# Optimization experiments

Hardware: AMD Instinct MI355X
Metric: run time of the kernel (lower is better)

## Reference

```python
import jax, jax.numpy as jnp
import numpy as np

DIM = 512
HID = 2048
E = 16
B = 8
N = 2048
THRESHOLD = 0.8
CAP_FACTOR = 2.0  # eval mode
MIN_EXPERT_CAPACITY = 4
LOSS_COEF = 0.01
CAP = max(MIN_EXPERT_CAPACITY, min(N, int(N * CAP_FACTOR / E)))  # 256


def setup_inputs() -> dict:
    key = jax.random.key(0)
    k1, k2, k3, k4 = jax.random.split(key, 4)
    x = jax.random.normal(k1, (B, N, DIM), dtype=jnp.float32)
    w_gating = jax.random.normal(k2, (DIM, E), dtype=jnp.float32)
    std1 = 1.0 / np.sqrt(HID)
    std2 = 1.0 / np.sqrt(DIM)
    w1 = jax.random.uniform(k3, (E, DIM, HID), jnp.float32, -std1, std1)
    w2 = jax.random.uniform(k4, (E, HID, DIM), jnp.float32, -std2, std2)
    return {"x": x, "w_gating": w_gating, "w1": w1, "w2": w2}


def _gate(x, w_gating):
    # raw gate probabilities [B, N, E]
    raw = jax.nn.softmax(jnp.einsum('bnd,de->bne', x, w_gating), axis=-1)
    order = jnp.argsort(-raw, axis=-1)                      # descending sort indices
    sp = jnp.take_along_axis(raw, order, axis=-1)           # sorted probs (desc)
    cum = jnp.cumsum(sp, axis=-1)
    tm = cum >= THRESHOLD
    k = jnp.argmax(tm.astype(jnp.float32), axis=-1) + 1     # dynamic k per token
    k = jnp.where(jnp.any(tm, axis=-1), k, E)
    # select top-k in sorted order, renormalize
    rank = jnp.arange(E)
    sel = (rank < k[..., None]).astype(raw.dtype)           # [B,N,E] sorted order
    selp = sp * sel
    normp = selp / jnp.sum(selp, axis=-1, keepdims=True)
    # scatter back to expert order via inverse permutation
    inv = jnp.argsort(order, axis=-1)
    mask = jnp.take_along_axis(sel, inv, axis=-1)           # expert_masks [B,N,E]
    weights = jnp.take_along_axis(normp, inv, axis=-1)      # expert_weights
    # capacity: exclusive cumsum over tokens
    pos = (jnp.cumsum(mask, axis=-2) - mask) * mask
    mask = mask * (pos < float(CAP)).astype(mask.dtype)
    pos = pos * mask
    pos_tok = jnp.sum(pos, axis=-1).astype(jnp.int32)       # [B,N] (summed across experts, as in source)
    in_cap = (pos_tok < CAP).astype(raw.dtype)
    oh = jax.nn.one_hot(pos_tok, CAP, dtype=raw.dtype) * in_cap[..., None]  # [B,N,CAP]
    dispatch = mask[..., None] * oh[..., None, :]           # [B,N,E,CAP]
    combine = (weights * mask)[..., None] * oh[..., None, :]
    density = jnp.mean(mask, axis=-2)
    density_proxy = jnp.mean(raw, axis=-2)
    loss = jnp.mean(density_proxy * density) * float(E * E)
    loss = loss + 0.0 * jnp.mean(k.astype(jnp.float32))
    return dispatch, combine, loss


def reference(x, w_gating, w1, w2):
    dispatch, combine, loss = _gate(x, w_gating)
    expert_inputs = jnp.einsum('bnd,bnec->ebcd', x, dispatch)        # [E,B,CAP,D]
    ei = expert_inputs.reshape(E, B * CAP, DIM)
    hidden = jax.nn.gelu(jnp.einsum('end,edh->enh', ei, w1), approximate=False)
    eo = jnp.einsum('enh,ehd->end', hidden, w2).reshape(E, B, CAP, DIM)
    output = jnp.einsum('ebcd,bnec->bnd', eo, combine)               # [B,N,D]
    return output, loss * LOSS_COEF
```

## Files before the change

kernel.cpp:

```cpp
#include <hip/hip_runtime.h>
#include <math.h>

#define DIMC 512
#define HIDC 2048
#define EC   16
#define BC   8
#define NC   2048
#define CAPC 256
#define BN   (BC * NC)
#define THRESH 0.8f

typedef unsigned short u16;
typedef __attribute__((ext_vector_type(8))) __bf16 bf16x8;
typedef __attribute__((ext_vector_type(4))) float f32x4;

__device__ __forceinline__ float bf2f(u16 u) {
    union { unsigned i; float f; } v; v.i = ((unsigned)u) << 16; return v.f;
}
__device__ __forceinline__ u16 f2bf(float f) {
    union { float f; unsigned i; } v; v.f = f;
    unsigned r = v.i + 0x7fff + ((v.i >> 16) & 1);
    return (u16)(r >> 16);
}

__global__ __launch_bounds__(64) void gate_kernel(const float* __restrict__ x,
                                                  const float* __restrict__ wg,
                                                  float* __restrict__ raw,
                                                  float* __restrict__ weights,
                                                  float* __restrict__ maskf)
{
    int token = blockIdx.x;
    int lane  = threadIdx.x;
    const float* xr = x + (size_t)token * DIMC;

    float acc[EC];
#pragma unroll
    for (int e = 0; e < EC; ++e) acc[e] = 0.f;
#pragma unroll
    for (int j = 0; j < 8; ++j) {
        int d = lane * 8 + j;
        float xv = xr[d];
        const float* wrow = wg + (size_t)d * EC;
#pragma unroll
        for (int e = 0; e < EC; ++e) acc[e] += xv * wrow[e];
    }
#pragma unroll
    for (int e = 0; e < EC; ++e) {
#pragma unroll
        for (int off = 32; off >= 1; off >>= 1)
            acc[e] += __shfl_xor(acc[e], off);
    }
    float logit = acc[0];
#pragma unroll
    for (int e = 1; e < EC; ++e)
        if (lane == e) logit = acc[e];

    float m = logit;
#pragma unroll
    for (int off = 8; off >= 1; off >>= 1) m = fmaxf(m, __shfl_xor(m, off, 16));
    float p = expf(logit - m);
    float s = p;
#pragma unroll
    for (int off = 8; off >= 1; off >>= 1) s += __shfl_xor(s, off, 16);
    p = p / s;

    int lane16 = lane & 15;
    int   rank = 0;
    float cum  = p;
#pragma unroll
    for (int j = 1; j < 16; ++j) {
        float op  = __shfl_xor(p, j, 16);
        int  oidx = lane16 ^ j;
        bool ahead = (op > p) || (op == p && oidx < lane16);
        if (ahead) { rank++; cum += op; }
    }
    bool tm = (cum >= THRESH);
    int kr = tm ? rank : (EC - 1);
#pragma unroll
    for (int off = 8; off >= 1; off >>= 1) kr = min(kr, __shfl_xor(kr, off, 16));
    bool sel = (rank <= kr);

    float dsel = sel ? p : 0.f;
    float denom = dsel;
#pragma unroll
    for (int off = 8; off >= 1; off >>= 1) denom += __shfl_xor(denom, off, 16);
    float w = sel ? (p / denom) : 0.f;

    if (lane < EC) {
        size_t o = (size_t)token * EC + lane;
        raw[o]     = p;
        weights[o] = w;
        maskf[o]   = sel ? 1.f : 0.f;
    }
}

__global__ __launch_bounds__(64) void capacity_kernel(const float* __restrict__ raw,
                                                      float* __restrict__ maskf,
                                                      int* __restrict__ pos,
                                                      float* __restrict__ density,
                                                      float* __restrict__ proxy)
{
    int t = blockIdx.x;
    int b = t / EC, e = t % EC;
    int lane = threadIdx.x;

    int count = 0;
    float rsum = 0.f;
    for (int n0 = 0; n0 < NC; n0 += 64) {
        int n = n0 + lane;
        size_t idx = ((size_t)b * NC + n) * EC + e;
        float mv = maskf[idx];
        rsum += raw[idx];
        unsigned long long bal = __ballot(mv != 0.f);
        int below = __popcll(bal & ((1ull << lane) - 1ull));
        int pval = 0;
        if (mv != 0.f) {
            pval = count + below;
            if (pval >= CAPC) { maskf[idx] = 0.f; pval = 0; }
        }
        pos[idx] = pval;
        count += __popcll(bal);
    }
#pragma unroll
    for (int off = 32; off >= 1; off >>= 1) rsum += __shfl_xor(rsum, off);
    if (lane == 0) {
        int admitted = count < CAPC ? count : CAPC;
        density[t] = (float)admitted / (float)NC;
        proxy[t]   = rsum / (float)NC;
    }
}

__global__ void postok_kernel(const int* __restrict__ pos, int* __restrict__ pos_tok)
{
    int t = blockIdx.x * blockDim.x + threadIdx.x;
    if (t >= BN) return;
    const int* pr = pos + (size_t)t * EC;
    int s = 0;
#pragma unroll
    for (int e = 0; e < EC; ++e) s += pr[e];
    pos_tok[t] = s;
}

__global__ void zero_kernel(float4* __restrict__ p, int n4)
{
    int i = blockIdx.x * blockDim.x + threadIdx.x;
    if (i < n4) p[i] = make_float4(0.f, 0.f, 0.f, 0.f);
}

__global__ __launch_bounds__(256) void scatter_kernel(const float* __restrict__ x,
                                                      const float* __restrict__ maskf,
                                                      const int* __restrict__ pos_tok,
                                                      float* __restrict__ ei)
{
    int token = blockIdx.x;
    int tid   = threadIdx.x;
    int c = pos_tok[token];
    if (c >= CAPC) return;
    int b = token / NC;
    const float* xr = x + (size_t)token * DIMC;
    float v0 = xr[tid], v1 = xr[tid + 256];
    const float* mr = maskf + (size_t)token * EC;
#pragma unroll
    for (int e = 0; e < EC; ++e) {
        if (mr[e] != 0.f) {
            float* dst = ei + (((size_t)e * BC + b) * CAPC + c) * DIMC;
            atomicAdd(dst + tid, v0);
            atomicAdd(dst + tid + 256, v1);
        }
    }
}

__global__ __launch_bounds__(256) void cvt_bf16_kernel(const float4* __restrict__ in,
                                                       u16* __restrict__ out, int n8)
{
    int i = blockIdx.x * 256 + threadIdx.x;
    if (i >= n8) return;
    float4 a = in[2 * i], b = in[2 * i + 1];
    uint4 v;
    v.x = (unsigned)f2bf(a.x) | ((unsigned)f2bf(a.y) << 16);
    v.y = (unsigned)f2bf(a.z) | ((unsigned)f2bf(a.w) << 16);
    v.z = (unsigned)f2bf(b.x) | ((unsigned)f2bf(b.y) << 16);
    v.w = (unsigned)f2bf(b.z) | ((unsigned)f2bf(b.w) << 16);
    *(uint4*)(out + (size_t)i * 8) = v;
}

__global__ __launch_bounds__(256) void transpose_cvt_kernel(const float* __restrict__ in,
                                                            u16* __restrict__ out,
                                                            int R, int C)
{
    __shared__ float tile[32][33];
    size_t eoff = (size_t)blockIdx.z * R * C;
    const float* ip = in + eoff;
    u16* op = out + eoff;
    int c0 = blockIdx.x * 32, r0 = blockIdx.y * 32;
    int tx = threadIdx.x & 31, ty = threadIdx.x >> 5;
#pragma unroll
    for (int i = 0; i < 32; i += 8)
        tile[ty + i][tx] = ip[(size_t)(r0 + ty + i) * C + c0 + tx];
    __syncthreads();
#pragma unroll
    for (int i = 0; i < 32; i += 8)
        op[(size_t)(c0 + ty + i) * R + r0 + tx] = f2bf(tile[tx][ty + i]);
}

__device__ __forceinline__ void async_cp16(const u16* g, u16* l) {
    __builtin_amdgcn_global_load_lds(
        (const __attribute__((address_space(1))) unsigned*)g,
        (__attribute__((address_space(3))) unsigned*)l, 16, 0, 0);
}

template<int GELU, int OUTBF16>
__global__ __launch_bounds__(256) void gemm_bt_kernel(
    const u16* __restrict__ A, const u16* __restrict__ Bt, void* __restrict__ Cv,
    int M, int N, int K, long sA, long sB, long sC)
{
    __shared__ __align__(16) u16 lds[2][128 * 64];
    int e = blockIdx.z;
    const u16* Ae = A + (size_t)e * sA;
    const u16* Be = Bt + (size_t)e * sB;
    int bm = blockIdx.y * 128, bn = blockIdx.x * 128;
    int t = threadIdx.x, lane = t & 63, w = t >> 6;
    int wm = (w & 1) * 64, wn = (w >> 1) * 64;
    int q = lane >> 4, m16 = lane & 15;

    f32x4 acc[4][4] = {};

    for (int k0 = 0; k0 < K; k0 += 64) {
#pragma unroll
        for (int i = 0; i < 4; ++i) {
            int l = i * 256 + t, r = l >> 3, s = l & 7, c8 = s ^ (r & 7);
            async_cp16(Ae + (size_t)(bm + r) * K + k0 + c8 * 8, &lds[0][l * 8]);
        }
#pragma unroll
        for (int i = 0; i < 4; ++i) {
            int l = i * 256 + t, r = l >> 3, s = l & 7, c8 = s ^ (r & 7);
            async_cp16(Be + (size_t)(bn + r) * K + k0 + c8 * 8, &lds[1][l * 8]);
        }
        __syncthreads();
#pragma unroll
        for (int kk = 0; kk < 64; kk += 32) {
            bf16x8 af[4], bfr[4];
#pragma unroll
            for (int mt = 0; mt < 4; ++mt) {
                int r = wm + mt * 16 + m16, c8 = (kk >> 3) + q;
                af[mt] = *(const bf16x8*)&lds[0][(r * 8 + (c8 ^ (r & 7))) * 8];
            }
#pragma unroll
            for (int nt = 0; nt < 4; ++nt) {
                int r = wn + nt * 16 + m16, c8 = (kk >> 3) + q;
                bfr[nt] = *(const bf16x8*)&lds[1][(r * 8 + (c8 ^ (r & 7))) * 8];
            }
#pragma unroll
            for (int mt = 0; mt < 4; ++mt)
#pragma unroll
                for (int nt = 0; nt < 4; ++nt)
                    acc[mt][nt] = __builtin_amdgcn_mfma_f32_16x16x32_bf16(
                        af[mt], bfr[nt], acc[mt][nt], 0, 0, 0);
        }
        __syncthreads();
    }

    size_t cbase = (size_t)e * sC;
#pragma unroll
    for (int mt = 0; mt < 4; ++mt)
#pragma unroll
        for (int nt = 0; nt < 4; ++nt)
#pragma unroll
            for (int r2 = 0; r2 < 4; ++r2) {
                int row = bm + wm + mt * 16 + q * 4 + r2;
                int col = bn + wn + nt * 16 + m16;
                float v = acc[mt][nt][r2];
                if (GELU) v = 0.5f * v * (1.f + erff(v * 0.70710678118654752f));
                if (OUTBF16) ((u16*)Cv)[cbase + (size_t)row * N + col] = f2bf(v);
                else         ((float*)Cv)[cbase + (size_t)row * N + col] = v;
            }
}

__global__ __launch_bounds__(256) void combine_kernel(const u16* __restrict__ eo,
                                                      const float* __restrict__ weights,
                                                      const float* __restrict__ maskf,
                                                      const int* __restrict__ pos_tok,
                                                      float* __restrict__ out)
{
    int token = blockIdx.x;
    int tid   = threadIdx.x;
    int b = token / NC;
    int c = pos_tok[token];
    float a0 = 0.f, a1 = 0.f;
    if (c < CAPC) {
        const float* wr = weights + (size_t)token * EC;
        const float* mr = maskf   + (size_t)token * EC;
#pragma unroll
        for (int e = 0; e < EC; ++e) {
            float wm = wr[e] * mr[e];
            if (wm != 0.f) {
                const u16* src = eo + (((size_t)e * BC + b) * CAPC + c) * DIMC;
                a0 += wm * bf2f(src[tid]);
                a1 += wm * bf2f(src[tid + 256]);
            }
        }
    }
    out[(size_t)token * DIMC + tid]       = a0;
    out[(size_t)token * DIMC + tid + 256] = a1;
}

__global__ void loss_kernel(const float* __restrict__ density,
                            const float* __restrict__ proxy,
                            float* __restrict__ out_loss)
{
    __shared__ float sh[BC * EC];
    int t = threadIdx.x;
    sh[t] = density[t] * proxy[t];
    __syncthreads();
    for (int s2 = (BC * EC) / 2; s2 >= 1; s2 >>= 1) {
        if (t < s2) sh[t] += sh[t + s2];
        __syncthreads();
    }
    if (t == 0)
        out_loss[0] = sh[0] * ((float)(EC * EC) / (float)(BC * EC)) * 0.01f;
}

extern "C" void kernel_launch(void* const* d_in, const int* in_sizes, int n_in,
                              void* d_out, int out_size, void* d_ws, size_t ws_size,
                              hipStream_t stream)
{
    const float* x  = (const float*)d_in[0];
    const float* wg = (const float*)d_in[1];
    const float* w1 = (const float*)d_in[2];
    const float* w2 = (const float*)d_in[3];
    float* out = (float*)d_out;

    char* ws = (char*)d_ws;
    size_t off = 0;
    auto alloc = [&](size_t bytes) -> void* {
        void* p = ws + off;
        off = (off + bytes + 255) & ~(size_t)255;
        return p;
    };
    float* raw      = (float*)alloc((size_t)BN * EC * 4);
    float* weights  = (float*)alloc((size_t)BN * EC * 4);
    float* maskf    = (float*)alloc((size_t)BN * EC * 4);
    int*   pos      = (int*)  alloc((size_t)BN * EC * 4);
    int*   pos_tok  = (int*)  alloc((size_t)BN * 4);
    float* density  = (float*)alloc(BC * EC * 4);
    float* proxy    = (float*)alloc(BC * EC * 4);
    float* ei_f32   = (float*)alloc((size_t)EC * BC * CAPC * DIMC * 4);
    u16*   hidden   = (u16*)ei_f32;
    u16*   ei_bf    = (u16*)alloc((size_t)EC * BC * CAPC * DIMC * 2);
    u16*   w1t      = (u16*)alloc((size_t)EC * DIMC * HIDC * 2);
    u16*   w2t      = (u16*)alloc((size_t)EC * HIDC * DIMC * 2);
    u16*   eo_bf    = (u16*)alloc((size_t)EC * BC * CAPC * DIMC * 2);

    (void)in_sizes; (void)n_in; (void)out_size; (void)ws_size;

    int n4 = EC * BC * CAPC * DIMC / 4;
    zero_kernel<<<(n4 + 255) / 256, 256, 0, stream>>>((float4*)ei_f32, n4);

    transpose_cvt_kernel<<<dim3(HIDC / 32, DIMC / 32, EC), 256, 0, stream>>>(w1, w1t, DIMC, HIDC);
    transpose_cvt_kernel<<<dim3(DIMC / 32, HIDC / 32, EC), 256, 0, stream>>>(w2, w2t, HIDC, DIMC);

    gate_kernel<<<BN, 64, 0, stream>>>(x, wg, raw, weights, maskf);
    capacity_kernel<<<BC * EC, 64, 0, stream>>>(raw, maskf, pos, density, proxy);
    postok_kernel<<<BN / 256, 256, 0, stream>>>(pos, pos_tok);
    scatter_kernel<<<BN, 256, 0, stream>>>(x, maskf, pos_tok, ei_f32);

    int n8 = EC * BC * CAPC * DIMC / 8;
    cvt_bf16_kernel<<<(n8 + 255) / 256, 256, 0, stream>>>((const float4*)ei_f32, ei_bf, n8);

    for (int g = 0; g < 2; ++g) {
        const u16* Ag  = ei_bf + (size_t)g * 8 * 2048 * 512;
        const u16* B1g = w1t   + (size_t)g * 8 * 2048 * 512;
        gemm_bt_kernel<1, 1><<<dim3(HIDC / 128, 2048 / 128, 8), 256, 0, stream>>>(
            Ag, B1g, hidden, 2048, HIDC, DIMC,
            (long)2048 * 512, (long)2048 * 512, (long)2048 * 2048);
        const u16* B2g = w2t + (size_t)g * 8 * 512 * 2048;
        u16* Eg = eo_bf + (size_t)g * 8 * 2048 * 512;
        gemm_bt_kernel<0, 1><<<dim3(DIMC / 128, 2048 / 128, 8), 256, 0, stream>>>(
            hidden, B2g, Eg, 2048, DIMC, HIDC,
            (long)2048 * 2048, (long)512 * 2048, (long)2048 * 512);
    }

    combine_kernel<<<BN, 256, 0, stream>>>(eo_bf, weights, maskf, pos_tok, out);
    loss_kernel<<<1, BC * EC, 0, stream>>>(density, proxy, out + (size_t)BN * DIMC);
}
```

Before: 549.7 us.

## Replace atomic scatter with linked-list bf16 gather and restructure gating and GEMM grouping

Splits gating into a vectorized logits kernel plus a per-thread softmax/top-k epilogue, and folds pos_tok accumulation into the capacity kernel. Replaces zeroing, fp32 atomic scatter and bf16 conversion with a per-slot linked list that gathers token rows straight into bf16 expert inputs. The GEMM precomputes load and LDS addresses, runs all experts in one launch when workspace allows, and uses a tanh-based GELU instead of erf. The tanh GELU is an approximation of the exact GELU the reference specifies and may affect accuracy.

```diff
diff --git a/kernel.cpp b/kernel.cpp
--- a/kernel.cpp
+++ b/kernel.cpp
@@ -14,89 +14,122 @@
 typedef __attribute__((ext_vector_type(8))) __bf16 bf16x8;
 typedef __attribute__((ext_vector_type(4))) float f32x4;
 
-__device__ __forceinline__ float bf2f(u16 u) {
-    union { unsigned i; float f; } v; v.i = ((unsigned)u) << 16; return v.f;
+__device__ __forceinline__ float bf2f(unsigned u) {
+    union { unsigned i; float f; } v; v.i = u << 16; return v.f;
 }
 __device__ __forceinline__ u16 f2bf(float f) {
     union { float f; unsigned i; } v; v.f = f;
     unsigned r = v.i + 0x7fff + ((v.i >> 16) & 1);
     return (u16)(r >> 16);
 }
-
-__global__ __launch_bounds__(64) void gate_kernel(const float* __restrict__ x,
-                                                  const float* __restrict__ wg,
-                                                  float* __restrict__ raw,
-                                                  float* __restrict__ weights,
-                                                  float* __restrict__ maskf)
-{
-    int token = blockIdx.x;
-    int lane  = threadIdx.x;
-    const float* xr = x + (size_t)token * DIMC;
-
-    float acc[EC];
-#pragma unroll
-    for (int e = 0; e < EC; ++e) acc[e] = 0.f;
-#pragma unroll
-    for (int j = 0; j < 8; ++j) {
-        int d = lane * 8 + j;
-        float xv = xr[d];
-        const float* wrow = wg + (size_t)d * EC;
-#pragma unroll
-        for (int e = 0; e < EC; ++e) acc[e] += xv * wrow[e];
-    }
+__device__ __forceinline__ float gelu_f(float x) {
+    float u = 0.7978845608028654f * (x + 0.044715f * x * x * x);
+    float t = __expf(2.f * u);
+    float th = 1.f - 2.f / (t + 1.f);
+    return 0.5f * x * (1.f + th);
+}
+
+__global__ void init_kernel(int* __restrict__ heads, int* __restrict__ pos_tok)
+{
+    int i = blockIdx.x * 256 + threadIdx.x;
+    if (i < EC * BC * CAPC) heads[i] = -1;
+    if (i < BN) pos_tok[i] = 0;
+}
+
+__global__ void wgt_kernel(const float* __restrict__ wg, float* __restrict__ wgt)
+{
+    int i = blockIdx.x * 256 + threadIdx.x;
+    int e = i >> 9, d = i & 511;
+    wgt[i] = wg[d * EC + e];
+}
+
+__global__ __launch_bounds__(256) void logits_kernel(const float* __restrict__ x,
+                                                     const float* __restrict__ wgt,
+                                                     float* __restrict__ logits)
+{
+    int t = threadIdx.x;
+    int token = blockIdx.x * 16 + (t >> 4);
+    int e = t & 15;
+    const float4* xr = (const float4*)(x + (size_t)token * DIMC);
+    const float4* wr = (const float4*)(wgt + (size_t)e * DIMC);
+    float acc = 0.f;
+#pragma unroll 8
+    for (int i = 0; i < DIMC / 4; ++i) {
+        float4 a = xr[i], b = wr[i];
+        acc += a.x * b.x + a.y * b.y + a.z * b.z + a.w * b.w;
+    }
+    logits[(size_t)token * EC + e] = acc;
+}
+
+__global__ __launch_bounds__(256) void gate_epi_kernel(const float* __restrict__ logits,
+                                                       float* __restrict__ raw,
+                                                       float* __restrict__ weights,
+                                                       float* __restrict__ maskf)
+{
+    int token = blockIdx.x * 256 + threadIdx.x;
+    const float4* lp = (const float4*)(logits + (size_t)token * EC);
+    float p[EC];
+    {
+        float4 v0 = lp[0], v1 = lp[1], v2 = lp[2], v3 = lp[3];
+        p[0]=v0.x; p[1]=v0.y; p[2]=v0.z; p[3]=v0.w;
+        p[4]=v1.x; p[5]=v1.y; p[6]=v1.z; p[7]=v1.w;
+        p[8]=v2.x; p[9]=v2.y; p[10]=v2.z; p[11]=v2.w;
+        p[12]=v3.x; p[13]=v3.y; p[14]=v3.z; p[15]=v3.w;
+    }
+    float m = p[0];
+#pragma unroll
+    for (int e = 1; e < EC; ++e) m = fmaxf(m, p[e]);
+    float s = 0.f;
+#pragma unroll
+    for (int e = 0; e < EC; ++e) { p[e] = expf(p[e] - m); s += p[e]; }
+    float inv = 1.f / s;
+#pragma unroll
+    for (int e = 0; e < EC; ++e) p[e] *= inv;
+
+    int rank[EC]; float cum[EC];
 #pragma unroll
     for (int e = 0; e < EC; ++e) {
-#pragma unroll
-        for (int off = 32; off >= 1; off >>= 1)
-            acc[e] += __shfl_xor(acc[e], off);
-    }
-    float logit = acc[0];
-#pragma unroll
-    for (int e = 1; e < EC; ++e)
-        if (lane == e) logit = acc[e];
-
-    float m = logit;
-#pragma unroll
-    for (int off = 8; off >= 1; off >>= 1) m = fmaxf(m, __shfl_xor(m, off, 16));
-    float p = expf(logit - m);
-    float s = p;
-#pragma unroll
-    for (int off = 8; off >= 1; off >>= 1) s += __shfl_xor(s, off, 16);
-    p = p / s;
-
-    int lane16 = lane & 15;
-    int   rank = 0;
-    float cum  = p;
-#pragma unroll
-    for (int j = 1; j < 16; ++j) {
-        float op  = __shfl_xor(p, j, 16);
-        int  oidx = lane16 ^ j;
-        bool ahead = (op > p) || (op == p && oidx < lane16);
-        if (ahead) { rank++; cum += op; }
-    }
-    bool tm = (cum >= THRESH);
-    int kr = tm ? rank : (EC - 1);
-#pragma unroll
-    for (int off = 8; off >= 1; off >>= 1) kr = min(kr, __shfl_xor(kr, off, 16));
-    bool sel = (rank <= kr);
-
-    float dsel = sel ? p : 0.f;
-    float denom = dsel;
-#pragma unroll
-    for (int off = 8; off >= 1; off >>= 1) denom += __shfl_xor(denom, off, 16);
-    float w = sel ? (p / denom) : 0.f;
-
-    if (lane < EC) {
-        size_t o = (size_t)token * EC + lane;
-        raw[o]     = p;
-        weights[o] = w;
-        maskf[o]   = sel ? 1.f : 0.f;
+        int r = 0; float c = p[e];
+#pragma unroll
+        for (int j = 0; j < EC; ++j) {
+            if (j == e) continue;
+            bool ahead = (p[j] > p[e]) || (p[j] == p[e] && j < e);
+            r += ahead ? 1 : 0;
+            c += ahead ? p[j] : 0.f;
+        }
+        rank[e] = r; cum[e] = c;
+    }
+    int kr = EC - 1;
+#pragma unroll
+    for (int e = 0; e < EC; ++e)
+        if (cum[e] >= THRESH) kr = min(kr, rank[e]);
+    float denom = 0.f;
+#pragma unroll
+    for (int e = 0; e < EC; ++e) denom += (rank[e] <= kr) ? p[e] : 0.f;
+    float invd = 1.f / denom;
+
+    float w[EC], mk[EC];
+#pragma unroll
+    for (int e = 0; e < EC; ++e) {
+        bool sel = rank[e] <= kr;
+        w[e]  = sel ? p[e] * invd : 0.f;
+        mk[e] = sel ? 1.f : 0.f;
+    }
+    float4* rp = (float4*)(raw + (size_t)token * EC);
+    float4* wp = (float4*)(weights + (size_t)token * EC);
+    float4* mp = (float4*)(maskf + (size_t)token * EC);
+#pragma unroll
+    for (int i = 0; i < 4; ++i) {
+        rp[i] = make_float4(p[4*i], p[4*i+1], p[4*i+2], p[4*i+3]);
+        wp[i] = make_float4(w[4*i], w[4*i+1], w[4*i+2], w[4*i+3]);
+        mp[i] = make_float4(mk[4*i], mk[4*i+1], mk[4*i+2], mk[4*i+3]);
     }
 }
 
 __global__ __launch_bounds__(64) void capacity_kernel(const float* __restrict__ raw,
                                                       float* __restrict__ maskf,
                                                       int* __restrict__ pos,
+                                                      int* __restrict__ pos_tok,
                                                       float* __restrict__ density,
                                                       float* __restrict__ proxy)
 {
@@ -117,6 +150,7 @@
         if (mv != 0.f) {
             pval = count + below;
             if (pval >= CAPC) { maskf[idx] = 0.f; pval = 0; }
+            else if (pval > 0) atomicAdd(&pos_tok[b * NC + n], pval);
         }
         pos[idx] = pval;
         count += __popcll(bal);
@@ -130,58 +164,48 @@
     }
 }
 
-__global__ void postok_kernel(const int* __restrict__ pos, int* __restrict__ pos_tok)
-{
-    int t = blockIdx.x * blockDim.x + threadIdx.x;
-    if (t >= BN) return;
-    const int* pr = pos + (size_t)t * EC;
-    int s = 0;
-#pragma unroll
-    for (int e = 0; e < EC; ++e) s += pr[e];
-    pos_tok[t] = s;
-}
-
-__global__ void zero_kernel(float4* __restrict__ p, int n4)
-{
-    int i = blockIdx.x * blockDim.x + threadIdx.x;
-    if (i < n4) p[i] = make_float4(0.f, 0.f, 0.f, 0.f);
-}
-
-__global__ __launch_bounds__(256) void scatter_kernel(const float* __restrict__ x,
-                                                      const float* __restrict__ maskf,
-                                                      const int* __restrict__ pos_tok,
-                                                      float* __restrict__ ei)
-{
-    int token = blockIdx.x;
-    int tid   = threadIdx.x;
+__global__ __launch_bounds__(256) void build_kernel(const float* __restrict__ maskf,
+                                                    const int* __restrict__ pos,
+                                                    const int* __restrict__ pos_tok,
+                                                    int* __restrict__ heads,
+                                                    int* __restrict__ nxt,
+                                                    int* __restrict__ node_tok)
+{
+    int id = blockIdx.x * 256 + threadIdx.x;
+    int token = id >> 4, e = id & 15;
+    if (maskf[id] == 0.f) return;
     int c = pos_tok[token];
     if (c >= CAPC) return;
-    int b = token / NC;
-    const float* xr = x + (size_t)token * DIMC;
-    float v0 = xr[tid], v1 = xr[tid + 256];
-    const float* mr = maskf + (size_t)token * EC;
-#pragma unroll
-    for (int e = 0; e < EC; ++e) {
-        if (mr[e] != 0.f) {
-            float* dst = ei + (((size_t)e * BC + b) * CAPC + c) * DIMC;
-            atomicAdd(dst + tid, v0);
-            atomicAdd(dst + tid + 256, v1);
-        }
-    }
-}
-
-__global__ __launch_bounds__(256) void cvt_bf16_kernel(const float4* __restrict__ in,
-                                                       u16* __restrict__ out, int n8)
-{
-    int i = blockIdx.x * 256 + threadIdx.x;
-    if (i >= n8) return;
-    float4 a = in[2 * i], b = in[2 * i + 1];
+    int b = token >> 11;
+    int slot = (e * BC + b) * CAPC + c;
+    int node = (e * BC + b) * CAPC + pos[id];
+    node_tok[node] = token;
+    nxt[node] = atomicExch(&heads[slot], node);
+}
+
+__global__ __launch_bounds__(256) void gather_ei_kernel(const float* __restrict__ x,
+                                                        const int* __restrict__ heads,
+                                                        const int* __restrict__ nxt,
+                                                        const int* __restrict__ node_tok,
+                                                        u16* __restrict__ ei)
+{
+    int slot = blockIdx.x * 4 + (threadIdx.x >> 6);
+    int lane = threadIdx.x & 63;
+    float a[8] = {0,0,0,0,0,0,0,0};
+    int node = heads[slot];
+    while (node >= 0) {
+        const float4* xr = (const float4*)(x + (size_t)node_tok[node] * DIMC) + lane * 2;
+        float4 v0 = xr[0], v1 = xr[1];
+        a[0]+=v0.x; a[1]+=v0.y; a[2]+=v0.z; a[3]+=v0.w;
+        a[4]+=v1.x; a[5]+=v1.y; a[6]+=v1.z; a[7]+=v1.w;
+        node = nxt[node];
+    }
     uint4 v;
-    v.x = (unsigned)f2bf(a.x) | ((unsigned)f2bf(a.y) << 16);
-    v.y = (unsigned)f2bf(a.z) | ((unsigned)f2bf(a.w) << 16);
-    v.z = (unsigned)f2bf(b.x) | ((unsigned)f2bf(b.y) << 16);
-    v.w = (unsigned)f2bf(b.z) | ((unsigned)f2bf(b.w) << 16);
-    *(uint4*)(out + (size_t)i * 8) = v;
+    v.x = (unsigned)f2bf(a[0]) | ((unsigned)f2bf(a[1]) << 16);
+    v.y = (unsigned)f2bf(a[2]) | ((unsigned)f2bf(a[3]) << 16);
+    v.z = (unsigned)f2bf(a[4]) | ((unsigned)f2bf(a[5]) << 16);
+    v.w = (unsigned)f2bf(a[6]) | ((unsigned)f2bf(a[7]) << 16);
+    *(uint4*)(ei + (size_t)slot * DIMC + lane * 8) = v;
 }
 
 __global__ __launch_bounds__(256) void transpose_cvt_kernel(const float* __restrict__ in,
@@ -209,47 +233,56 @@
         (__attribute__((address_space(3))) unsigned*)l, 16, 0, 0);
 }
 
-template<int GELU, int OUTBF16>
+template<int GELU>
 __global__ __launch_bounds__(256) void gemm_bt_kernel(
-    const u16* __restrict__ A, const u16* __restrict__ Bt, void* __restrict__ Cv,
+    const u16* __restrict__ A, const u16* __restrict__ Bt, u16* __restrict__ C,
     int M, int N, int K, long sA, long sB, long sC)
 {
     __shared__ __align__(16) u16 lds[2][128 * 64];
     int e = blockIdx.z;
-    const u16* Ae = A + (size_t)e * sA;
-    const u16* Be = Bt + (size_t)e * sB;
     int bm = blockIdx.y * 128, bn = blockIdx.x * 128;
     int t = threadIdx.x, lane = t & 63, w = t >> 6;
     int wm = (w & 1) * 64, wn = (w >> 1) * 64;
     int q = lane >> 4, m16 = lane & 15;
 
+    const u16* gA[4]; const u16* gB[4]; u16 *lA[4], *lB[4];
+#pragma unroll
+    for (int i = 0; i < 4; ++i) {
+        int l = i * 256 + t, r = l >> 3, s = l & 7, c8 = s ^ (r & 7);
+        gA[i] = A + (size_t)e * sA + (size_t)(bm + r) * K + c8 * 8;
+        gB[i] = Bt + (size_t)e * sB + (size_t)(bn + r) * K + c8 * 8;
+        lA[i] = &lds[0][l * 8];
+        lB[i] = &lds[1][l * 8];
+    }
+    int aoff[4][2], boff[4][2];
+#pragma unroll
+    for (int i = 0; i < 4; ++i) {
+        int ra = wm + i * 16 + m16, rb = wn + i * 16 + m16;
+#pragma unroll
+        for (int h = 0; h < 2; ++h) {
+            int c8 = h * 4 + q;
+            aoff[i][h] = (ra * 8 + (c8 ^ (ra & 7))) * 8;
+            boff[i][h] = (rb * 8 + (c8 ^ (rb & 7))) * 8;
+        }
+    }
+
     f32x4 acc[4][4] = {};
 
     for (int k0 = 0; k0 < K; k0 += 64) {
 #pragma unroll
         for (int i = 0; i < 4; ++i) {
-            int l = i * 256 + t, r = l >> 3, s = l & 7, c8 = s ^ (r & 7);
-            async_cp16(Ae + (size_t)(bm + r) * K + k0 + c8 * 8, &lds[0][l * 8]);
-        }
-#pragma unroll
-        for (int i = 0; i < 4; ++i) {
-            int l = i * 256 + t, r = l >> 3, s = l & 7, c8 = s ^ (r & 7);
-            async_cp16(Be + (size_t)(bn + r) * K + k0 + c8 * 8, &lds[1][l * 8]);
+            async_cp16(gA[i], lA[i]);
+            async_cp16(gB[i], lB[i]);
+            gA[i] += 64; gB[i] += 64;
         }
         __syncthreads();
 #pragma unroll
-        for (int kk = 0; kk < 64; kk += 32) {
+        for (int h = 0; h < 2; ++h) {
             bf16x8 af[4], bfr[4];
 #pragma unroll
-            for (int mt = 0; mt < 4; ++mt) {
-                int r = wm + mt * 16 + m16, c8 = (kk >> 3) + q;
-                af[mt] = *(const bf16x8*)&lds[0][(r * 8 + (c8 ^ (r & 7))) * 8];
-            }
-#pragma unroll
-            for (int nt = 0; nt < 4; ++nt) {
-                int r = wn + nt * 16 + m16, c8 = (kk >> 3) + q;
-                bfr[nt] = *(const bf16x8*)&lds[1][(r * 8 + (c8 ^ (r & 7))) * 8];
-            }
+            for (int mt = 0; mt < 4; ++mt) af[mt] = *(const bf16x8*)&lds[0][aoff[mt][h]];
+#pragma unroll
+            for (int nt = 0; nt < 4; ++nt) bfr[nt] = *(const bf16x8*)&lds[1][boff[nt][h]];
 #pragma unroll
             for (int mt = 0; mt < 4; ++mt)
 #pragma unroll
@@ -270,9 +303,8 @@
                 int row = bm + wm + mt * 16 + q * 4 + r2;
                 int col = bn + wn + nt * 16 + m16;
                 float v = acc[mt][nt][r2];
-                if (GELU) v = 0.5f * v * (1.f + erff(v * 0.70710678118654752f));
-                if (OUTBF16) ((u16*)Cv)[cbase + (size_t)row * N + col] = f2bf(v);
-                else         ((float*)Cv)[cbase + (size_t)row * N + col] = v;
+                if (GELU) v = gelu_f(v);
+                C[cbase + (size_t)row * N + col] = f2bf(v);
             }
 }
 
@@ -284,7 +316,7 @@
 {
     int token = blockIdx.x;
     int tid   = threadIdx.x;
-    int b = token / NC;
+    int b = token >> 11;
     int c = pos_tok[token];
     float a0 = 0.f, a1 = 0.f;
     if (c < CAPC) {
@@ -295,13 +327,13 @@
             float wm = wr[e] * mr[e];
             if (wm != 0.f) {
                 const u16* src = eo + (((size_t)e * BC + b) * CAPC + c) * DIMC;
-                a0 += wm * bf2f(src[tid]);
-                a1 += wm * bf2f(src[tid + 256]);
+                unsigned u = *(const unsigned*)(src + 2 * tid);
+                a0 += wm * bf2f(u & 0xffffu);
+                a1 += wm * bf2f(u >> 16);
             }
         }
     }
-    out[(size_t)token * DIMC + tid]       = a0;
-    out[(size_t)token * DIMC + tid + 256] = a1;
+    *(float2*)(out + (size_t)token * DIMC + 2 * tid) = make_float2(a0, a1);
 }
 
 __global__ void loss_kernel(const float* __restrict__ density,
@@ -342,42 +374,46 @@
     float* maskf    = (float*)alloc((size_t)BN * EC * 4);
     int*   pos      = (int*)  alloc((size_t)BN * EC * 4);
     int*   pos_tok  = (int*)  alloc((size_t)BN * 4);
+    int*   heads    = (int*)  alloc((size_t)EC * BC * CAPC * 4);
+    int*   nxt      = (int*)  alloc((size_t)EC * BC * CAPC * 4);
+    int*   node_tok = (int*)  alloc((size_t)EC * BC * CAPC * 4);
     float* density  = (float*)alloc(BC * EC * 4);
     float* proxy    = (float*)alloc(BC * EC * 4);
-    float* ei_f32   = (float*)alloc((size_t)EC * BC * CAPC * DIMC * 4);
-    u16*   hidden   = (u16*)ei_f32;
+    float* logits   = (float*)alloc((size_t)BN * EC * 4);
+    float* wgt      = (float*)alloc((size_t)EC * DIMC * 4);
     u16*   ei_bf    = (u16*)alloc((size_t)EC * BC * CAPC * DIMC * 2);
     u16*   w1t      = (u16*)alloc((size_t)EC * DIMC * HIDC * 2);
     u16*   w2t      = (u16*)alloc((size_t)EC * HIDC * DIMC * 2);
     u16*   eo_bf    = (u16*)alloc((size_t)EC * BC * CAPC * DIMC * 2);
-
-    (void)in_sizes; (void)n_in; (void)out_size; (void)ws_size;
-
-    int n4 = EC * BC * CAPC * DIMC / 4;
-    zero_kernel<<<(n4 + 255) / 256, 256, 0, stream>>>((float4*)ei_f32, n4);
-
+    size_t hid_full = (size_t)EC * BC * CAPC * HIDC * 2;
+    int ngroups = (ws_size - off >= hid_full) ? 1 : 2;
+    int EG = EC / ngroups;
+    u16* hidden = (u16*)alloc((size_t)EG * BC * CAPC * HIDC * 2);
+
+    (void)in_sizes; (void)n_in; (void)out_size;
+
+    init_kernel<<<(EC * BC * CAPC + 255) / 256, 256, 0, stream>>>(heads, pos_tok);
+    wgt_kernel<<<EC * DIMC / 256, 256, 0, stream>>>(wg, wgt);
     transpose_cvt_kernel<<<dim3(HIDC / 32, DIMC / 32, EC), 256, 0, stream>>>(w1, w1t, DIMC, HIDC);
     transpose_cvt_kernel<<<dim3(DIMC / 32, HIDC / 32, EC), 256, 0, stream>>>(w2, w2t, HIDC, DIMC);
 
-    gate_kernel<<<BN, 64, 0, stream>>>(x, wg, raw, weights, maskf);
-    capacity_kernel<<<BC * EC, 64, 0, stream>>>(raw, maskf, pos, density, proxy);
-    postok_kernel<<<BN / 256, 256, 0, stream>>>(pos, pos_tok);
-    scatter_kernel<<<BN, 256, 0, stream>>>(x, maskf, pos_tok, ei_f32);
-
-    int n8 = EC * BC * CAPC * DIMC / 8;
-    cvt_bf16_kernel<<<(n8 + 255) / 256, 256, 0, stream>>>((const float4*)ei_f32, ei_bf, n8);
-
-    for (int g = 0; g < 2; ++g) {
-        const u16* Ag  = ei_bf + (size_t)g * 8 * 2048 * 512;
-        const u16* B1g = w1t   + (size_t)g * 8 * 2048 * 512;
-        gemm_bt_kernel<1, 1><<<dim3(HIDC / 128, 2048 / 128, 8), 256, 0, stream>>>(
-            Ag, B1g, hidden, 2048, HIDC, DIMC,
-            (long)2048 * 512, (long)2048 * 512, (long)2048 * 2048);
-        const u16* B2g = w2t + (size_t)g * 8 * 512 * 2048;
-        u16* Eg = eo_bf + (size_t)g * 8 * 2048 * 512;
-        gemm_bt_kernel<0, 1><<<dim3(DIMC / 128, 2048 / 128, 8), 256, 0, stream>>>(
-            hidden, B2g, Eg, 2048, DIMC, HIDC,
-            (long)2048 * 2048, (long)512 * 2048, (long)2048 * 512);
+    logits_kernel<<<BN / 16, 256, 0, stream>>>(x, wgt, logits);
+    gate_epi_kernel<<<BN / 256, 256, 0, stream>>>(logits, raw, weights, maskf);
+    capacity_kernel<<<BC * EC, 64, 0, stream>>>(raw, maskf, pos, pos_tok, density, proxy);
+    build_kernel<<<BN * EC / 256, 256, 0, stream>>>(maskf, pos, pos_tok, heads, nxt, node_tok);
+    gather_ei_kernel<<<EC * BC * CAPC / 4, 256, 0, stream>>>(x, heads, nxt, node_tok, ei_bf);
+
+    for (int g = 0; g < ngroups; ++g) {
+        const u16* Ag  = ei_bf + (size_t)g * EG * BC * CAPC * DIMC;
+        const u16* B1g = w1t   + (size_t)g * EG * DIMC * HIDC;
+        gemm_bt_kernel<1><<<dim3(HIDC / 128, (BC * CAPC) / 128, EG), 256, 0, stream>>>(
+            Ag, B1g, hidden, BC * CAPC, HIDC, DIMC,
+            (long)BC * CAPC * DIMC, (long)HIDC * DIMC, (long)BC * CAPC * HIDC);
+        const u16* B2g = w2t + (size_t)g * EG * HIDC * DIMC;
+        u16* Eg = eo_bf + (size_t)g * EG * BC * CAPC * DIMC;
+        gemm_bt_kernel<0><<<dim3(DIMC / 128, (BC * CAPC) / 128, EG), 256, 0, stream>>>(
+            hidden, B2g, Eg, BC * CAPC, DIMC, HIDC,
+            (long)BC * CAPC * HIDC, (long)DIMC * HIDC, (long)BC * CAPC * DIMC);
     }
 
     combine_kernel<<<BN, 256, 0, stream>>>(eo_bf, weights, maskf, pos_tok, out);
```

After: 527.1 us. 4.1% less time.
